# Optimization experiments

Hardware: AMD Instinct MI355X
Metric: run time of the kernel (lower is better)

## Reference

```python
import jax, jax.numpy as jnp
import numpy as np

NQ, NK, D = 8192, 8192, 256
NEG_INF = -1e30


def setup_inputs() -> dict:
    key = jax.random.key(0)
    kK, kV, kQ, kM = jax.random.split(key, 4)
    K = jax.random.normal(kK, (NK, D), dtype=jnp.float32)
    V = jax.random.normal(kV, (NK, D), dtype=jnp.float32)
    Q = jax.random.normal(kQ, (NQ, D), dtype=jnp.float32)
    m = jax.random.randint(kM, (NQ, NK), 0, 2) > 0  # bool mask, True = attend
    return {"K": K, "V": V, "Q": Q, "m": m}


def reference(K, V, Q, m):
    # affinity: scaled dot product with optional mask
    scale = 1.0 / jnp.sqrt(jnp.asarray(D, dtype=Q.dtype))
    QKt = jnp.einsum('qd,kd->qk', Q, K) * scale  # [NQ, NK]
    QKt = jnp.where(m, QKt, NEG_INF)
    # normalization: softmax over keys
    QKt_n = jax.nn.softmax(QKt, axis=-1)
    # weighted sum of values
    return QKt_n @ V  # [NQ, D]
```

## Files before the change

kernel.cpp:

```cpp
#include <hip/hip_runtime.h>
#include <stdint.h>
#include <stddef.h>

#define NQS 8192
#define NKS 8192
#define DS  256

typedef _Float16 half8 __attribute__((ext_vector_type(8)));
typedef _Float16 half4v __attribute__((ext_vector_type(4)));
typedef float floatx16 __attribute__((ext_vector_type(16)));

#define MFMA32(A,B,C) __builtin_amdgcn_mfma_f32_32x32x16_f16(A,B,C,0,0,0)

#define GLOAD_LDS16(gp, lp) \
  __builtin_amdgcn_global_load_lds((const __attribute__((address_space(1))) void*)(gp), \
                                   (__attribute__((address_space(3))) void*)(lp), 16, 0, 0)

#define TILE_ELEMS 16384
#define SUB_ELEMS  8192

__global__ void detect_mask(const uint4* __restrict__ M, uint32_t* __restrict__ flag){
  __shared__ uint32_t s[256];
  uint32_t acc = 0;
  for (int i = threadIdx.x; i < 4096; i += 256){
    uint4 v = M[i];
    acc |= v.x | v.y | v.z | v.w;
  }
  s[threadIdx.x] = acc;
  __syncthreads();
  if (threadIdx.x == 0){
    uint32_t t = 0;
    for (int i = 0; i < 256; i++) t |= s[i];
    *flag = (t > 1u) ? 1u : 0u;
  }
}

__global__ void prep(const float* __restrict__ Qf, const float* __restrict__ K,
                     const float* __restrict__ V, const uint8_t* __restrict__ M8,
                     const uint32_t* __restrict__ flag,
                     _Float16* __restrict__ Qh, _Float16* __restrict__ Kc,
                     _Float16* __restrict__ Vc, uint32_t* __restrict__ Mp2){
  const int tid = threadIdx.x;
  if (blockIdx.x < 1024){
    size_t u = (size_t)blockIdx.x*256 + tid;
    const float4* src = (const float4*)(Qf + u*8);
    float4 a = src[0], b = src[1];
    half8 h = {(_Float16)a.x,(_Float16)a.y,(_Float16)a.z,(_Float16)a.w,
               (_Float16)b.x,(_Float16)b.y,(_Float16)b.z,(_Float16)b.w};
    *(half8*)(Qh + u*8) = h;
  } else if (blockIdx.x < 2048){
    int gid = (blockIdx.x - 1024)*256 + tid;
    int key = gid & 8191;
    int c   = gid >> 13;
    int kt = c >> 1, t = c & 1;
    const float4* s = (const float4*)(K + (size_t)key*DS + kt*16 + t*8);
    float4 x = s[0], y = s[1];
    half8 h = {(_Float16)x.x,(_Float16)x.y,(_Float16)x.z,(_Float16)x.w,
               (_Float16)y.x,(_Float16)y.y,(_Float16)y.z,(_Float16)y.w};
    int tile = key >> 6, mt = (key >> 5) & 1, k32 = key & 31;
    size_t off = (size_t)tile*TILE_ELEMS + (((mt*16 + kt)*2 + t)*32 + k32)*8;
    *(half8*)(Kc + off) = h;
  } else if (blockIdx.x < 3072){
    int gid = (blockIdx.x - 2048)*256 + tid;
    int d32 = gid & 31;
    int t   = (gid >> 5) & 1;
    int nt  = (gid >> 6) & 7;
    int kkt = (gid >> 9) & 3;
    int tile = gid >> 11;
    int d = nt*32 + d32;
    int kb8 = tile*64 + kkt*16 + t*8;
    half8 h;
    #pragma unroll
    for (int j=0;j<8;j++) h[j] = (_Float16)V[(size_t)(kb8 + j)*DS + d];
    *(half8*)(Vc + (size_t)gid*8) = h;
  } else {
    const int bi  = blockIdx.x - 3072;
    const int bgr = bi >> 4;
    const int bgw = bi & 15;
    const int r   = (bgr << 6) + (tid & 63);
    const int wl  = tid >> 6;
    const bool by = (*flag != 0u);
    #pragma unroll
    for (int i = 0; i < 4; ++i){
      const int w = (bgw << 4) + i*4 + wl;
      uint32_t word = 0;
      if (by){
        const uint4* p = (const uint4*)(M8 + (size_t)r*8192 + w*32);
        uint4 a = p[0], b = p[1];
        uint32_t v[8] = {a.x,a.y,a.z,a.w,b.x,b.y,b.z,b.w};
        #pragma unroll
        for (int q=0;q<8;q++){
          word |= (((v[q]      ) & 0xFFu) ? 1u:0u) << (q*4+0);
          word |= (((v[q] >>  8) & 0xFFu) ? 1u:0u) << (q*4+1);
          word |= (((v[q] >> 16) & 0xFFu) ? 1u:0u) << (q*4+2);
          word |= (((v[q] >> 24)        ) ? 1u:0u) << (q*4+3);
        }
      } else {
        const uint4* p = (const uint4*)M8 + (size_t)r*2048 + w*8;
        #pragma unroll
        for (int q=0;q<8;q++){
          uint4 v = p[q];
          word |= (v.x?1u:0u) << (q*4+0);
          word |= (v.y?1u:0u) << (q*4+1);
          word |= (v.z?1u:0u) << (q*4+2);
          word |= (v.w?1u:0u) << (q*4+3);
        }
      }
      Mp2[(size_t)w*NQS + r] = word;
    }
  }
}

__global__ __launch_bounds__(256, 2) void attn_fwd(
  const _Float16* __restrict__ Qh, const _Float16* __restrict__ Kc,
  const _Float16* __restrict__ Vc, const uint32_t* __restrict__ Mp2,
  _Float16* __restrict__ Oph, float* __restrict__ Lo)
{
  __shared__ _Float16 Kls[2][SUB_ELEMS];
  __shared__ _Float16 Vls[2][SUB_ELEMS];

  const int tid  = threadIdx.x;
  const int w    = tid >> 6;
  const int lane = tid & 63;
  const int q32  = lane & 31;
  const int t    = lane >> 5;
  const int b    = blockIdx.x;
  const int kh   = b & 7;
  const int rowbase = (b >> 3)*128 + w*32;
  const int sub0 = kh << 5;
  const int kw0  = kh << 5;

  const float kLog = 0.09016844005556021f;
  const float MFIX = 6.0f;

  half8 qf[16];
  {
    const _Float16* qrow = Qh + (size_t)(rowbase + q32)*DS;
    #pragma unroll
    for (int kt=0;kt<16;kt++)
      qf[kt] = *(const half8*)(qrow + kt*16 + t*8);
  }

  floatx16 O[8];
  #pragma unroll
  for (int nt=0;nt<8;nt++)
    #pragma unroll
    for (int i=0;i<16;i++) O[nt][i] = 0.f;
  float lsum = 0.f;

  {
    const size_t base = (size_t)sub0 * SUB_ELEMS;
    #pragma unroll
    for (int j=0;j<4;j++){
      int c = w*4 + j;
      GLOAD_LDS16(Kc + base + c*512 + lane*8, &Kls[0][c*512]);
      GLOAD_LDS16(Vc + base + c*512 + lane*8, &Vls[0][c*512]);
    }
  }
  uint32_t mcur = Mp2[(size_t)kw0*NQS + rowbase + q32];
  __syncthreads();

  #pragma unroll 1
  for (int it=0; it<32; ++it){
    const int buf = it & 1;

    uint32_t mnext = 0u;
    if (it < 31){
      const size_t base = (size_t)(sub0 + it + 1) * SUB_ELEMS;
      #pragma unroll
      for (int j=0;j<4;j++){
        int c = w*4 + j;
        GLOAD_LDS16(Kc + base + c*512 + lane*8, &Kls[buf^1][c*512]);
        GLOAD_LDS16(Vc + base + c*512 + lane*8, &Vls[buf^1][c*512]);
      }
      mnext = Mp2[(size_t)(kw0 + it + 1)*NQS + rowbase + q32];
    }
    const uint32_t mw = mcur;

    floatx16 S0, S1;
    #pragma unroll
    for (int i=0;i<16;i++){ S0[i]=0.f; S1[i]=0.f; }
    #pragma unroll
    for (int kt=0;kt<8;kt++){
      half8 kA = *(const half8*)&Kls[buf][((kt*2 + t)*32 + q32)*8];
      S0 = MFMA32(kA, qf[kt], S0);
    }
    #pragma unroll
    for (int kt=8;kt<16;kt++){
      half8 kA = *(const half8*)&Kls[buf][((kt*2 + t)*32 + q32)*8];
      S1 = MFMA32(kA, qf[kt], S1);
    }

    uint32_t pk[4][2];
    #pragma unroll
    for (int s=0;s<4;s++){
      float pv[4];
      #pragma unroll
      for (int rr=0;rr<4;rr++){
        int i = s*4 + rr;
        int keybit = rr + 8*s + 4*t;
        float e = __builtin_amdgcn_exp2f(__builtin_fmaf(S0[i]+S1[i], kLog, -MFIX));
        float p = ((mw >> keybit) & 1u) ? e : 0.f;
        lsum += p;
        pv[rr] = p;
      }
      pk[s][0] = __builtin_bit_cast(uint32_t, __builtin_amdgcn_cvt_pkrtz(pv[0], pv[1]));
      pk[s][1] = __builtin_bit_cast(uint32_t, __builtin_amdgcn_cvt_pkrtz(pv[2], pv[3]));
    }

    #pragma unroll
    for (int kt2=0; kt2<2; ++kt2){
      const int s_own  = kt2*2 + t;
      const int s_send = kt2*2 + (t^1);
      uint32_t r0 = __shfl_xor(__builtin_bit_cast(int, pk[s_send][0]), 32);
      uint32_t r1 = __shfl_xor(__builtin_bit_cast(int, pk[s_send][1]), 32);
      uint32_t lo0 = (t==0) ? pk[s_own][0] : r0;
      uint32_t lo1 = (t==0) ? pk[s_own][1] : r1;
      uint32_t hi0 = (t==0) ? r0 : pk[s_own][0];
      uint32_t hi1 = (t==0) ? r1 : pk[s_own][1];
      uint4 u = {lo0, lo1, hi0, hi1};
      half8 pa = __builtin_bit_cast(half8, u);
      #pragma unroll
      for (int nt=0;nt<8;nt++){
        half8 vB = *(const half8*)&Vls[buf][(((kt2*8+nt)*2 + t)*32 + q32)*8];
        O[nt] = MFMA32(pa, vB, O[nt]);
      }
    }

    mcur = mnext;
    __syncthreads();
  }

  lsum += __builtin_bit_cast(float, __shfl_xor(__builtin_bit_cast(int, lsum), 32));
  if (t == 0) Lo[(size_t)b*128 + w*32 + q32] = lsum;

  _Float16* ob = Oph + ((size_t)b*128 + w*32)*256;
  #pragma unroll
  for (int nt=0;nt<8;nt++){
    #pragma unroll
    for (int i=0;i<16;i++){
      int row = (i&3) + 8*(i>>2) + 4*t;
      ob[(size_t)row*256 + nt*32 + q32] = (_Float16)O[nt][i];
    }
  }
}

__global__ void combine8(const _Float16* __restrict__ Oph, const float* __restrict__ Lo,
                         float* __restrict__ Out){
  int gid = blockIdx.x*256 + threadIdx.x;
  int row = gid >> 6;
  int c4  = (gid & 63) << 2;
  int g   = row >> 7, r = row & 127;

  float lt = 0.f;
  #pragma unroll
  for (int kh=0;kh<8;kh++) lt += Lo[(size_t)(g*8 + kh)*128 + r];
  float li = 1.0f / lt;

  float4 acc = {0,0,0,0};
  #pragma unroll
  for (int kh=0;kh<8;kh++){
    half4v o = *(const half4v*)(Oph + ((size_t)(g*8 + kh)*128 + r)*256 + c4);
    acc.x += (float)o[0]; acc.y += (float)o[1];
    acc.z += (float)o[2]; acc.w += (float)o[3];
  }
  acc.x *= li; acc.y *= li; acc.z *= li; acc.w *= li;
  *(float4*)(Out + (size_t)row*DS + c4) = acc;
}

extern "C" void kernel_launch(void* const* d_in, const int* in_sizes, int n_in,
                              void* d_out, int out_size, void* d_ws, size_t ws_size,
                              hipStream_t stream){
  (void)in_sizes; (void)n_in; (void)out_size; (void)ws_size;
  const float*   K = (const float*)d_in[0];
  const float*   V = (const float*)d_in[1];
  const float*   Q = (const float*)d_in[2];
  const uint8_t* M = (const uint8_t*)d_in[3];
  float* Out = (float*)d_out;

  _Float16* Qh  = (_Float16*)d_ws;
  _Float16* Kc  = Qh + (size_t)NQS*DS;
  _Float16* Vc  = Kc + (size_t)NKS*DS;
  uint32_t* Mp2 = (uint32_t*)(Vc + (size_t)NKS*DS);
  _Float16* Oph = (_Float16*)(Mp2 + (size_t)256*NQS);
  float*    Lo  = (float*)(Oph + (size_t)512*128*256);
  uint32_t* flag = (uint32_t*)(Lo + 512*128);

  hipLaunchKernelGGL(detect_mask, dim3(1),    dim3(256), 0, stream, (const uint4*)M, flag);
  hipLaunchKernelGGL(prep,        dim3(5120), dim3(256), 0, stream, Q, K, V, M, flag, Qh, Kc, Vc, Mp2);
  hipLaunchKernelGGL(attn_fwd,    dim3(512),  dim3(256), 0, stream, Qh, Kc, Vc, Mp2, Oph, Lo);
  hipLaunchKernelGGL(combine8,    dim3(2048), dim3(256), 0, stream, Oph, Lo, Out);
}
```

Baseline: 514.8 us.

## Fuse mask bit-packing into attention kernel via prefetched LDS nibble slabs

Removes the separate mask-packing pass from the prep kernel. The attention kernel now reads the raw mask slab for each key tile directly, prefetched one iteration ahead in registers, and packs it into per-row nibbles in a double-buffered LDS array. This avoids writing and re-reading the packed mask buffer in global memory. In exchange, each of the 8 key-splits reads its own mask region inside the main loop, which adds global load traffic, extra ALU packing work and register pressure in the hot loop.

```diff
diff --git a/kernel.cpp b/kernel.cpp
--- a/kernel.cpp
+++ b/kernel.cpp
@@ -36,10 +36,9 @@
 }
 
 __global__ void prep(const float* __restrict__ Qf, const float* __restrict__ K,
-                     const float* __restrict__ V, const uint8_t* __restrict__ M8,
-                     const uint32_t* __restrict__ flag,
+                     const float* __restrict__ V,
                      _Float16* __restrict__ Qh, _Float16* __restrict__ Kc,
-                     _Float16* __restrict__ Vc, uint32_t* __restrict__ Mp2){
+                     _Float16* __restrict__ Vc){
   const int tid = threadIdx.x;
   if (blockIdx.x < 1024){
     size_t u = (size_t)blockIdx.x*256 + tid;
@@ -60,7 +59,7 @@
     int tile = key >> 6, mt = (key >> 5) & 1, k32 = key & 31;
     size_t off = (size_t)tile*TILE_ELEMS + (((mt*16 + kt)*2 + t)*32 + k32)*8;
     *(half8*)(Kc + off) = h;
-  } else if (blockIdx.x < 3072){
+  } else {
     int gid = (blockIdx.x - 2048)*256 + tid;
     int d32 = gid & 31;
     int t   = (gid >> 5) & 1;
@@ -73,51 +72,52 @@
     #pragma unroll
     for (int j=0;j<8;j++) h[j] = (_Float16)V[(size_t)(kb8 + j)*DS + d];
     *(half8*)(Vc + (size_t)gid*8) = h;
+  }
+}
+
+struct MaskRegs { uint4 v[4]; };
+
+__device__ __forceinline__ void mask_slab_load(bool bm, const uint8_t* __restrict__ M8,
+                                               int rb, int k0, int tid, MaskRegs& m){
+  if (bm){
+    m.v[0] = *(const uint4*)(M8 + (size_t)(rb + (tid>>1))*NKS + k0 + (tid&1)*16);
   } else {
-    const int bi  = blockIdx.x - 3072;
-    const int bgr = bi >> 4;
-    const int bgw = bi & 15;
-    const int r   = (bgr << 6) + (tid & 63);
-    const int wl  = tid >> 6;
-    const bool by = (*flag != 0u);
-    #pragma unroll
-    for (int i = 0; i < 4; ++i){
-      const int w = (bgw << 4) + i*4 + wl;
-      uint32_t word = 0;
-      if (by){
-        const uint4* p = (const uint4*)(M8 + (size_t)r*8192 + w*32);
-        uint4 a = p[0], b = p[1];
-        uint32_t v[8] = {a.x,a.y,a.z,a.w,b.x,b.y,b.z,b.w};
-        #pragma unroll
-        for (int q=0;q<8;q++){
-          word |= (((v[q]      ) & 0xFFu) ? 1u:0u) << (q*4+0);
-          word |= (((v[q] >>  8) & 0xFFu) ? 1u:0u) << (q*4+1);
-          word |= (((v[q] >> 16) & 0xFFu) ? 1u:0u) << (q*4+2);
-          word |= (((v[q] >> 24)        ) ? 1u:0u) << (q*4+3);
-        }
-      } else {
-        const uint4* p = (const uint4*)M8 + (size_t)r*2048 + w*8;
-        #pragma unroll
-        for (int q=0;q<8;q++){
-          uint4 v = p[q];
-          word |= (v.x?1u:0u) << (q*4+0);
-          word |= (v.y?1u:0u) << (q*4+1);
-          word |= (v.z?1u:0u) << (q*4+2);
-          word |= (v.w?1u:0u) << (q*4+3);
-        }
-      }
-      Mp2[(size_t)w*NQS + r] = word;
+    const uint32_t* M32 = (const uint32_t*)M8;
+    #pragma unroll
+    for (int jj=0;jj<4;jj++)
+      m.v[jj] = *(const uint4*)(M32 + (size_t)(rb + jj*32 + (tid>>3))*NKS + k0 + (tid&7)*4);
+  }
+}
+__device__ __forceinline__ void mask_slab_pack(bool bm, int tid, const MaskRegs& m,
+                                               uint8_t (*__restrict__ nib)[8]){
+  if (bm){
+    const uint32_t* pv = (const uint32_t*)&m.v[0];
+    #pragma unroll
+    for (int q=0;q<4;q++){
+      uint32_t x = pv[q];
+      uint8_t nb = (uint8_t)(((x&0x000000FFu)?1u:0u)|((x&0x0000FF00u)?2u:0u)|
+                             ((x&0x00FF0000u)?4u:0u)|((x&0xFF000000u)?8u:0u));
+      nib[tid>>1][(tid&1)*4 + q] = nb;
+    }
+  } else {
+    #pragma unroll
+    for (int jj=0;jj<4;jj++){
+      uint4 x = m.v[jj];
+      uint8_t nb = (uint8_t)((x.x?1u:0u)|(x.y?2u:0u)|(x.z?4u:0u)|(x.w?8u:0u));
+      nib[jj*32 + (tid>>3)][tid&7] = nb;
     }
   }
 }
 
 __global__ __launch_bounds__(256, 2) void attn_fwd(
   const _Float16* __restrict__ Qh, const _Float16* __restrict__ Kc,
-  const _Float16* __restrict__ Vc, const uint32_t* __restrict__ Mp2,
-  _Float16* __restrict__ Oph, float* __restrict__ Lo)
+  const _Float16* __restrict__ Vc, const uint8_t* __restrict__ Msk,
+  const uint32_t* __restrict__ flag, _Float16* __restrict__ Oph,
+  float* __restrict__ Lo)
 {
   __shared__ _Float16 Kls[2][SUB_ELEMS];
   __shared__ _Float16 Vls[2][SUB_ELEMS];
+  __shared__ uint8_t  Nib[2][128][8];
 
   const int tid  = threadIdx.x;
   const int w    = tid >> 6;
@@ -126,12 +126,15 @@
   const int t    = lane >> 5;
   const int b    = blockIdx.x;
   const int kh   = b & 7;
-  const int rowbase = (b >> 3)*128 + w*32;
+  const int rb   = (b >> 3)*128;
+  const int rowbase = rb + w*32;
   const int sub0 = kh << 5;
-  const int kw0  = kh << 5;
+  const int kbase = kh << 10;
 
   const float kLog = 0.09016844005556021f;
   const float MFIX = 6.0f;
+
+  const bool bm = (*flag != 0u);
 
   half8 qf[16];
   {
@@ -156,15 +159,17 @@
       GLOAD_LDS16(Kc + base + c*512 + lane*8, &Kls[0][c*512]);
       GLOAD_LDS16(Vc + base + c*512 + lane*8, &Vls[0][c*512]);
     }
-  }
-  uint32_t mcur = Mp2[(size_t)kw0*NQS + rowbase + q32];
+    MaskRegs m0;
+    mask_slab_load(bm, Msk, rb, kbase, tid, m0);
+    mask_slab_pack(bm, tid, m0, Nib[0]);
+  }
   __syncthreads();
 
   #pragma unroll 1
   for (int it=0; it<32; ++it){
     const int buf = it & 1;
 
-    uint32_t mnext = 0u;
+    MaskRegs mpf;
     if (it < 31){
       const size_t base = (size_t)(sub0 + it + 1) * SUB_ELEMS;
       #pragma unroll
@@ -173,9 +178,14 @@
         GLOAD_LDS16(Kc + base + c*512 + lane*8, &Kls[buf^1][c*512]);
         GLOAD_LDS16(Vc + base + c*512 + lane*8, &Vls[buf^1][c*512]);
       }
-      mnext = Mp2[(size_t)(kw0 + it + 1)*NQS + rowbase + q32];
-    }
-    const uint32_t mw = mcur;
+      mask_slab_load(bm, Msk, rb, kbase + (it+1)*32, tid, mpf);
+    }
+
+    const uint2 nq = *(const uint2*)&Nib[buf][w*32 + q32][0];
+    const uint32_t nib_s[4] = { (nq.x >> (8*t))      & 0xFu,
+                                (nq.x >> (16 + 8*t)) & 0xFu,
+                                (nq.y >> (8*t))      & 0xFu,
+                                (nq.y >> (16 + 8*t)) & 0xFu };
 
     floatx16 S0, S1;
     #pragma unroll
@@ -198,9 +208,8 @@
       #pragma unroll
       for (int rr=0;rr<4;rr++){
         int i = s*4 + rr;
-        int keybit = rr + 8*s + 4*t;
         float e = __builtin_amdgcn_exp2f(__builtin_fmaf(S0[i]+S1[i], kLog, -MFIX));
-        float p = ((mw >> keybit) & 1u) ? e : 0.f;
+        float p = ((nib_s[s] >> rr) & 1u) ? e : 0.f;
         lsum += p;
         pv[rr] = p;
       }
@@ -227,7 +236,8 @@
       }
     }
 
-    mcur = mnext;
+    if (it < 31) mask_slab_pack(bm, tid, mpf, Nib[buf^1]);
+
     __syncthreads();
   }
 
@@ -281,13 +291,12 @@
   _Float16* Qh  = (_Float16*)d_ws;
   _Float16* Kc  = Qh + (size_t)NQS*DS;
   _Float16* Vc  = Kc + (size_t)NKS*DS;
-  uint32_t* Mp2 = (uint32_t*)(Vc + (size_t)NKS*DS);
-  _Float16* Oph = (_Float16*)(Mp2 + (size_t)256*NQS);
+  _Float16* Oph = Vc + (size_t)NKS*DS;
   float*    Lo  = (float*)(Oph + (size_t)512*128*256);
   uint32_t* flag = (uint32_t*)(Lo + 512*128);
 
   hipLaunchKernelGGL(detect_mask, dim3(1),    dim3(256), 0, stream, (const uint4*)M, flag);
-  hipLaunchKernelGGL(prep,        dim3(5120), dim3(256), 0, stream, Q, K, V, M, flag, Qh, Kc, Vc, Mp2);
-  hipLaunchKernelGGL(attn_fwd,    dim3(512),  dim3(256), 0, stream, Qh, Kc, Vc, Mp2, Oph, Lo);
+  hipLaunchKernelGGL(prep,        dim3(3072), dim3(256), 0, stream, Q, K, V, Qh, Kc, Vc);
+  hipLaunchKernelGGL(attn_fwd,    dim3(512),  dim3(256), 0, stream, Qh, Kc, Vc, M, flag, Oph, Lo);
   hipLaunchKernelGGL(combine8,    dim3(2048), dim3(256), 0, stream, Oph, Lo, Out);
 }
```

Measured after the change: 503.9 us. 2.1% less time.
